# Kernel optimization log

Measured on AMD Instinct MI355X. Metric: run time of the kernel, lower is better.

Reference implementation:

```python
import jax, jax.numpy as jnp
import numpy as np

N, E = 50000, 800000
IN_CH, INTER, H1, H2 = 256, 32, 8, 8
C2 = IN_CH // H2  # 32
NEG_SLOPE = 0.2


def setup_inputs() -> dict:
    key = jax.random.key(0)
    ks = jax.random.split(key, 10)
    x = jax.random.normal(ks[0], (N, IN_CH), dtype=jnp.float32)
    edge_index = jax.random.randint(ks[1], (2, E), 0, N, dtype=jnp.int32)
    s = 0.05
    W1 = jax.random.normal(ks[2], (H1 * INTER, IN_CH), dtype=jnp.float32) * s
    att_src1 = jax.random.normal(ks[3], (1, H1, INTER), dtype=jnp.float32) * s
    att_dst1 = jax.random.normal(ks[4], (1, H1, INTER), dtype=jnp.float32) * s
    b1 = jnp.zeros((H1 * INTER,), dtype=jnp.float32)
    W2 = jax.random.normal(ks[5], (H2 * C2, H1 * INTER), dtype=jnp.float32) * s
    att_src2 = jax.random.normal(ks[6], (1, H2, C2), dtype=jnp.float32) * s
    att_dst2 = jax.random.normal(ks[7], (1, H2, C2), dtype=jnp.float32) * s
    b2 = jnp.zeros((H2 * C2,), dtype=jnp.float32)
    return {"x": x, "edge_index": edge_index,
            "W1": W1, "att_src1": att_src1, "att_dst1": att_dst1, "b1": b1,
            "W2": W2, "att_src2": att_src2, "att_dst2": att_dst2, "b2": b2}


def gat_conv(x, edge_index, W, att_src, att_dst, bias, H, C):
    # PyG GATConv (shared lin for src/dst, add_self_loops=False, concat=True)
    n = x.shape[0]
    src, dst = edge_index[0], edge_index[1]
    xw = (x @ W.T).reshape(n, H, C)                     # [N,H,C]
    a_src = jnp.sum(xw * att_src, axis=-1)              # [N,H]
    a_dst = jnp.sum(xw * att_dst, axis=-1)              # [N,H]
    e = a_src[src] + a_dst[dst]                         # [E,H]
    e = jnp.where(e >= 0, e, NEG_SLOPE * e)             # LeakyReLU(0.2)
    # segment softmax over edges grouped by destination node
    m = jax.ops.segment_max(e, dst, num_segments=n)     # [N,H]
    ex = jnp.exp(e - m[dst])
    denom = jax.ops.segment_sum(ex, dst, num_segments=n)
    alpha = ex / (denom[dst] + 1e-16)                   # [E,H]
    # weighted scatter-aggregate of source messages
    msg = xw[src] * alpha[:, :, None]                   # [E,H,C]
    out = jax.ops.segment_sum(msg, dst, num_segments=n) # [N,H,C]
    return out.reshape(n, H * C) + bias


def reference(x, edge_index, W1, att_src1, att_dst1, b1, W2, att_src2, att_dst2, b2):
    h = gat_conv(x, edge_index, W1, att_src1, att_dst1, b1, H1, INTER)
    h = jax.nn.gelu(h, approximate=False)  # F.gelu default is exact
    h = gat_conv(h, edge_index, W2, att_src2, att_dst2, b2, H2, C2)
    return h[-1]  # eval-path super node
```

## Files before the change

### kernel.cpp

```cpp
#include <hip/hip_runtime.h>
#include <math.h>

#define N_NODES 50000
#define N_EDGES 800000
#define TGT     (N_NODES - 1)
#define C2MAX   256
#define KCAP    258
#define ELMAX   256
#define ROWS    (ELMAX + 1)
#define PBLK    8
#define SCANBLK 512
#define BCAP    8
#define BMWORDS 1568

struct WS {
  int* blkcnt2;
  int* blkbuf2;
  int* cnt2;
  int* fin_k;
  int* gfin;
  int* g_uniq;
  int* g_slot;
  int* g_misc;
  int* l1src;
  float* W1T4;
  float* W2T4;
  float* g_xw2;
  float* g_as2;
  float* g_ad2;
  float* g_as1;
  float* g_ad1;
  float* g_xw1;
};
__host__ __device__ inline WS carve(char* ws) {
  WS w; int* p = (int*)ws;
  w.blkcnt2 = p; p += SCANBLK;
  w.blkbuf2 = p; p += SCANBLK * BCAP;
  w.cnt2 = p;    p += 272;
  w.fin_k = p;   p += 272;
  w.gfin = p;    p += 16;
  w.g_uniq = p;  p += 272;
  w.g_slot = p;  p += C2MAX;
  w.g_misc = p;  p += 16;
  w.l1src = p;   p += KCAP * ELMAX;
  float* f = (float*)p;
  w.W1T4 = f;   f += 65536;
  w.W2T4 = f;   f += 65536;
  w.g_xw2 = f;  f += KCAP * 256;
  w.g_as2 = f;  f += KCAP * 8;
  w.g_ad2 = f;  f += KCAP * 8;
  w.g_as1 = f;  f += KCAP * ROWS * 8;
  w.g_ad1 = f;  f += KCAP * ROWS * 8;
  w.g_xw1 = f;
  return w;
}

__global__ __launch_bounds__(256) void k_scan2(const int* __restrict__ eidx,
    const float* __restrict__ W1, const float* __restrict__ W2, char* ws) {
  WS w = carve(ws);
  int t = threadIdx.x;
  __shared__ float lds[64][65];
  __shared__ int s_list[BCAP];
  __shared__ int s_n;
  if (t == 0) s_n = 0;
  if (blockIdx.x == 0)
    for (int i = t; i < 272 + 272 + 16; i += 256) w.cnt2[i] = 0;
  if (blockIdx.x < 32) {
    int m  = blockIdx.x >> 4;
    int ti = (blockIdx.x >> 2) & 3, tj = blockIdx.x & 3;
    const float* src = m ? W2 : W1;
    float*       dst = m ? w.W2T4 : w.W1T4;
    int r0 = t >> 6, cc = t & 63;
    float tmp[16];
#pragma unroll
    for (int p = 0; p < 16; ++p)
      tmp[p] = src[(ti * 64 + p * 4 + r0) * 256 + tj * 64 + cc];
#pragma unroll
    for (int p = 0; p < 16; ++p)
      lds[p * 4 + r0][cc] = tmp[p];
    __syncthreads();
    int c40 = t >> 6, o = t & 63;
#pragma unroll
    for (int p2 = 0; p2 < 4; ++p2) {
      int c4l = p2 * 4 + c40;
      float4 v = make_float4(lds[o][4 * c4l + 0], lds[o][4 * c4l + 1],
                             lds[o][4 * c4l + 2], lds[o][4 * c4l + 3]);
      ((float4*)dst)[(tj * 16 + c4l) * 256 + ti * 64 + o] = v;
    }
  }
  __syncthreads();
  int tid = blockIdx.x * 256 + t;
  int nthreads = gridDim.x * 256;
  const int* esrc = eidx;
  const int4* edst4 = (const int4*)(eidx + N_EDGES);
  for (int i = tid; i < N_EDGES / 4; i += nthreads) {
    int4 d = edst4[i];
    int dv[4] = {d.x, d.y, d.z, d.w};
#pragma unroll
    for (int j = 0; j < 4; ++j)
      if (dv[j] == TGT) {
        int p = atomicAdd(&s_n, 1);
        if (p < BCAP) s_list[p] = esrc[4 * i + j];
      }
  }
  __syncthreads();
  int n = min(s_n, BCAP);
  if (t == 0) w.blkcnt2[blockIdx.x] = n;
  if (t < n)  w.blkbuf2[blockIdx.x * BCAP + t] = s_list[t];
}

__global__ __launch_bounds__(256) void k_scan1(const int* __restrict__ eidx, char* ws) {
  WS w = carve(ws);
  int t = threadIdx.x;
  __shared__ int s_counts[SCANBLK];
  __shared__ int s_e[C2MAX], s_scan[256], s_uniq[KCAP], s_slot[C2MAX], s_kv[3];
  __shared__ unsigned s_bm[BMWORDS];
  for (int b = t; b < SCANBLK; b += 256) s_counts[b] = min(w.blkcnt2[b], BCAP);
  __syncthreads();
  for (int r = 0; r < SCANBLK / 256; ++r) {
    int b = r * 256 + t;
    int off = 0;
    for (int q = 0; q < b; ++q) off += s_counts[q];
    int n = s_counts[b];
    for (int j = 0; j < n; ++j)
      if (off + j < C2MAX) s_e[off + j] = w.blkbuf2[b * BCAP + j];
    if (b == SCANBLK - 1) s_kv[2] = min(off + n, C2MAX);
  }
  __syncthreads();
  int c2 = s_kv[2];
  int firstIdx = t;
  if (t < c2) {
    int s = s_e[t];
    for (int q = 0; q < t; ++q) if (s_e[q] == s) { firstIdx = q; break; }
  }
  s_scan[t] = (t < c2 && firstIdx == t) ? 1 : 0;
  __syncthreads();
  for (int off = 1; off < 256; off <<= 1) {
    int add = (t >= off) ? s_scan[t - off] : 0;
    __syncthreads();
    s_scan[t] += add;
    __syncthreads();
  }
  if (t < c2 && firstIdx == t) s_uniq[s_scan[t] - 1] = s_e[t];
  __syncthreads();
  if (t < c2) s_slot[t] = s_scan[firstIdx] - 1;
  if (t == 0) {
    int K1 = (c2 > 0) ? s_scan[255] : 0;
    int kd = -1;
    for (int i = 0; i < K1; ++i) if (s_uniq[i] == TGT) { kd = i; break; }
    if (kd < 0) { s_uniq[K1] = TGT; kd = K1; K1++; }
    s_kv[0] = K1; s_kv[1] = kd;
  }
  for (int i = t; i < BMWORDS; i += 256) s_bm[i] = 0u;
  __syncthreads();
  int K1 = s_kv[0];
  for (int i = t; i < K1; i += 256) {
    int u = s_uniq[i];
    atomicOr(&s_bm[u >> 5], 1u << (u & 31));
  }
  if (blockIdx.x == 0) {
    for (int i = t; i < K1; i += 256) w.g_uniq[i] = s_uniq[i];
    if (t < c2) w.g_slot[t] = s_slot[t];
    if (t == 0) { w.g_misc[0] = K1; w.g_misc[1] = s_kv[1]; w.g_misc[2] = c2; }
  }
  __syncthreads();
  int tid = blockIdx.x * 256 + t;
  int nthreads = gridDim.x * 256;
  const int* esrc = eidx;
  const int4* edst4 = (const int4*)(eidx + N_EDGES);
  for (int i = tid; i < N_EDGES / 4; i += nthreads) {
    int4 d = edst4[i];
    int dv[4] = {d.x, d.y, d.z, d.w};
#pragma unroll
    for (int j = 0; j < 4; ++j) {
      int u = dv[j];
      if ((s_bm[u >> 5] >> (u & 31)) & 1u) {
        int k = 0;
        for (int q = 0; q < K1; ++q) if (s_uniq[q] == u) { k = q; break; }
        int p = atomicAdd(&w.cnt2[k], 1);
        if (p < ELMAX) w.l1src[k * ELMAX + p] = esrc[4 * i + j];
      }
    }
  }
}

__global__ __launch_bounds__(256) void k_fused(const float* __restrict__ x,
    const float* __restrict__ aS1, const float* __restrict__ aD1,
    const float* __restrict__ b1, const float* __restrict__ aS2,
    const float* __restrict__ aD2, const float* __restrict__ b2,
    float* __restrict__ out, char* ws) {
  WS w = carve(ws);
  int K1 = w.g_misc[0];
  int k = blockIdx.x;
  if (k >= K1) return;
  int t = threadIdx.x;
  int ne = min(w.cnt2[k], ELMAX);
  int items = ne + 1;
  int myNode = w.g_uniq[k];
  __shared__ __align__(16) float s_xsT[4 * 256];
  __shared__ float s_redS[4 * 256], s_redD[4 * 256];
  __shared__ float s_as[ROWS * 8];
  __shared__ float s_p[ELMAX * 8];
  __shared__ float s_den[8];
  __shared__ __align__(16) float s_h1[256];
  __shared__ int   s_sl[C2MAX];
  __shared__ int   s_win;
  const float4* W1v = (const float4*)w.W1T4;
  const float4* W2v = (const float4*)w.W2T4;
  const float4* xsT4 = (const float4*)s_xsT;

  for (int b = blockIdx.y; b * 4 < items; b += PBLK) {
    int base = b * 4;
    int na = min(4, items - base);
    int nd[4];
#pragma unroll
    for (int i = 0; i < 4; ++i) {
      int it = base + i;
      nd[i] = (it < ne) ? w.l1src[k * ELMAX + it] : myNode;
    }
#pragma unroll
    for (int i = 0; i < 4; ++i)
      s_xsT[t * 4 + i] = x[(size_t)nd[i] * 256 + t];
    __syncthreads();
    float a0 = 0.f, a1 = 0.f, a2 = 0.f, a3 = 0.f;
    for (int cc = 0; cc < 64; cc += 8) {
      float4 wreg[8];
#pragma unroll
      for (int j = 0; j < 8; ++j)
        wreg[j] = W1v[(size_t)(cc + j) * 256 + t];
#pragma unroll
      for (int j = 0; j < 8; ++j) {
        float4 wv = wreg[j];
        int c4 = cc + j;
        float4 x0 = xsT4[4 * c4 + 0];
        float4 x1 = xsT4[4 * c4 + 1];
        float4 x2 = xsT4[4 * c4 + 2];
        float4 x3 = xsT4[4 * c4 + 3];
        a0 = fmaf(wv.x, x0.x, a0); a0 = fmaf(wv.y, x1.x, a0); a0 = fmaf(wv.z, x2.x, a0); a0 = fmaf(wv.w, x3.x, a0);
        a1 = fmaf(wv.x, x0.y, a1); a1 = fmaf(wv.y, x1.y, a1); a1 = fmaf(wv.z, x2.y, a1); a1 = fmaf(wv.w, x3.y, a1);
        a2 = fmaf(wv.x, x0.z, a2); a2 = fmaf(wv.y, x1.z, a2); a2 = fmaf(wv.z, x2.z, a2); a2 = fmaf(wv.w, x3.z, a2);
        a3 = fmaf(wv.x, x0.w, a3); a3 = fmaf(wv.y, x1.w, a3); a3 = fmaf(wv.z, x2.w, a3); a3 = fmaf(wv.w, x3.w, a3);
      }
    }
    float accs[4] = {a0, a1, a2, a3};
    for (int i = 0; i < na; ++i) {
      int it = base + i;
      int row = k * ROWS + it;
      if (it < ne)
        w.g_xw1[(size_t)row * 256 + t] = accs[i];
      s_redS[i * 256 + t] = accs[i] * aS1[t];
      s_redD[i * 256 + t] = accs[i] * aD1[t];
    }
    __syncthreads();
    if (t < 32) {
      int i = t >> 3, h = t & 7;
      if (i < na) {
        float s = 0.f, dd = 0.f;
        for (int q = 0; q < 32; ++q) {
          s  += s_redS[i * 256 + h * 32 + q];
          dd += s_redD[i * 256 + h * 32 + q];
        }
        int row = k * ROWS + base + i;
        w.g_as1[row * 8 + h] = s;
        w.g_ad1[row * 8 + h] = dd;
      }
    }
    __syncthreads();
  }

  __syncthreads();
  if (t == 0) {
    __threadfence();
    int old = __hip_atomic_fetch_add(&w.fin_k[k], 1, __ATOMIC_ACQ_REL, __HIP_MEMORY_SCOPE_AGENT);
    s_win = (old == PBLK - 1);
  }
  __syncthreads();
  if (!s_win) return;
  __threadfence();

  for (int i = t; i < items * 8; i += 256) s_as[i] = w.g_as1[(size_t)(k * ROWS) * 8 + i];
  __syncthreads();
  if (t < 8) {
    int h = t;
    float adst = w.g_ad1[(size_t)(k * ROWS + ne) * 8 + h];
    float m = -INFINITY;
    for (int j = 0; j < ne; ++j) {
      float e = s_as[j * 8 + h] + adst;
      e = (e >= 0.f) ? e : 0.2f * e;
      m = fmaxf(m, e);
    }
    float den = 0.f;
    for (int j = 0; j < ne; ++j) {
      float e = s_as[j * 8 + h] + adst;
      e = (e >= 0.f) ? e : 0.2f * e;
      float p = expf(e - m);
      s_p[j * 8 + h] = p;
      den += p;
    }
    s_den[h] = den + 1e-16f;
  }
  __syncthreads();
  int h = t >> 5;
  float acc = 0.f;
  const float* xwb = w.g_xw1 + (size_t)(k * ROWS) * 256 + t;
  for (int j0 = 0; j0 < ne; j0 += 8) {
    float tmp[8];
#pragma unroll
    for (int j = 0; j < 8; ++j)
      tmp[j] = (j0 + j < ne) ? xwb[(size_t)(j0 + j) * 256] : 0.f;
#pragma unroll
    for (int j = 0; j < 8; ++j)
      if (j0 + j < ne) acc = fmaf(s_p[(j0 + j) * 8 + h], tmp[j], acc);
  }
  float o = (ne > 0) ? acc / s_den[h] : 0.f;
  o += b1[t];
  s_h1[t] = 0.5f * o * (1.f + erff(o * 0.70710678118654752440f));
  __syncthreads();
  float a2s = 0.f;
  const float4* h1v = (const float4*)s_h1;
  for (int cc = 0; cc < 64; cc += 8) {
    float4 wreg[8];
#pragma unroll
    for (int j = 0; j < 8; ++j)
      wreg[j] = W2v[(size_t)(cc + j) * 256 + t];
#pragma unroll
    for (int j = 0; j < 8; ++j) {
      float4 wv = wreg[j];
      float4 hv = h1v[cc + j];
      a2s = fmaf(wv.x, hv.x, a2s); a2s = fmaf(wv.y, hv.y, a2s);
      a2s = fmaf(wv.z, hv.z, a2s); a2s = fmaf(wv.w, hv.w, a2s);
    }
  }
  w.g_xw2[k * 256 + t] = a2s;
  s_redS[t] = a2s * aS2[t];
  s_redD[t] = a2s * aD2[t];
  __syncthreads();
  if (t < 8) {
    float s = 0.f, dd = 0.f;
    for (int q = 0; q < 32; ++q) { s += s_redS[t * 32 + q]; dd += s_redD[t * 32 + q]; }
    w.g_as2[k * 8 + t] = s;
    w.g_ad2[k * 8 + t] = dd;
  }

  __syncthreads();
  if (t == 0) {
    __threadfence();
    int old = __hip_atomic_fetch_add(&w.gfin[0], 1, __ATOMIC_ACQ_REL, __HIP_MEMORY_SCOPE_AGENT);
    s_win = (old == K1 - 1);
  }
  __syncthreads();
  if (!s_win) return;
  __threadfence();

  int c2 = min(w.g_misc[2], C2MAX);
  int kd = w.g_misc[1];
  for (int j = t; j < c2; j += 256) s_sl[j] = w.g_slot[j];
  __syncthreads();
  if (t < 8) {
    float adst = w.g_ad2[kd * 8 + t];
    float m = -INFINITY;
    for (int j = 0; j < c2; ++j) {
      float e = w.g_as2[s_sl[j] * 8 + t] + adst;
      e = (e >= 0.f) ? e : 0.2f * e;
      m = fmaxf(m, e);
    }
    float den = 0.f;
    for (int j = 0; j < c2; ++j) {
      float e = w.g_as2[s_sl[j] * 8 + t] + adst;
      e = (e >= 0.f) ? e : 0.2f * e;
      float p = expf(e - m);
      s_p[j * 8 + t] = p;
      den += p;
    }
    s_den[t] = den + 1e-16f;
  }
  __syncthreads();
  float acc2 = 0.f;
  for (int j0 = 0; j0 < c2; j0 += 8) {
    float tmp[8];
#pragma unroll
    for (int j = 0; j < 8; ++j)
      tmp[j] = (j0 + j < c2) ? w.g_xw2[s_sl[j0 + j] * 256 + t] : 0.f;
#pragma unroll
    for (int j = 0; j < 8; ++j)
      if (j0 + j < c2) acc2 = fmaf(s_p[(j0 + j) * 8 + h], tmp[j], acc2);
  }
  float o2 = (c2 > 0) ? acc2 / s_den[h] : 0.f;
  out[t] = o2 + b2[t];
}

extern "C" void kernel_launch(void* const* d_in, const int* in_sizes, int n_in,
                              void* d_out, int out_size, void* d_ws, size_t ws_size,
                              hipStream_t stream) {
  const float* x    = (const float*)d_in[0];
  const int*   eidx = (const int*)d_in[1];
  const float* W1   = (const float*)d_in[2];
  const float* aS1  = (const float*)d_in[3];
  const float* aD1  = (const float*)d_in[4];
  const float* b1   = (const float*)d_in[5];
  const float* W2   = (const float*)d_in[6];
  const float* aS2  = (const float*)d_in[7];
  const float* aD2  = (const float*)d_in[8];
  const float* b2   = (const float*)d_in[9];
  float* out = (float*)d_out;
  char*  ws  = (char*)d_ws;

  k_scan2<<<SCANBLK, 256, 0, stream>>>(eidx, W1, W2, ws);
  k_scan1<<<SCANBLK, 256, 0, stream>>>(eidx, ws);
  k_fused<<<dim3(KCAP, PBLK), 256, 0, stream>>>(x, aS1, aD1, b1, aS2, aD2, b2, out, ws);
}
```

Baseline: 138.0 us.

## Shrink fused grid, parallel-scan block offsets, pad finish counters, relax atomics

Halves the scan grid to 256 blocks with a larger per-block buffer and replaces the serial per-thread prefix sum over block counts with a shared-memory parallel scan. It also shrinks the fused kernel grid from 258x8 to 96x5, pads the per-k finish counters to separate cache lines, and switches the completion atomics to relaxed ordering while keeping the explicit fences. The smaller grid only stays correct if the kernel loops over k beyond the grid size, which is not visible. The unguarded g_xw1 store writes padding rows, and relaxed atomics rely on the surrounding threadfences for ordering.

```diff
diff --git a/kernel.cpp b/kernel.cpp
--- a/kernel.cpp
+++ b/kernel.cpp
@@ -6,11 +6,13 @@
 #define TGT     (N_NODES - 1)
 #define C2MAX   256
 #define KCAP    258
+#define KGRID   96
 #define ELMAX   256
 #define ROWS    (ELMAX + 1)
-#define PBLK    8
-#define SCANBLK 512
-#define BCAP    8
+#define PBLK    5
+#define FINSTR  16
+#define SCANBLK 256
+#define BCAP    12
 #define BMWORDS 1568
 
 struct WS {
@@ -37,7 +39,7 @@
   w.blkcnt2 = p; p += SCANBLK;
   w.blkbuf2 = p; p += SCANBLK * BCAP;
   w.cnt2 = p;    p += 272;
-  w.fin_k = p;   p += 272;
+  w.fin_k = p;   p += KGRID * FINSTR;
   w.gfin = p;    p += 16;
   w.g_uniq = p;  p += 272;
   w.g_slot = p;  p += C2MAX;
@@ -54,6 +56,7 @@
   w.g_xw1 = f;
   return w;
 }
+#define NZERO (272 + KGRID * FINSTR + 16)
 
 __global__ __launch_bounds__(256) void k_scan2(const int* __restrict__ eidx,
     const float* __restrict__ W1, const float* __restrict__ W2, char* ws) {
@@ -64,7 +67,7 @@
   __shared__ int s_n;
   if (t == 0) s_n = 0;
   if (blockIdx.x == 0)
-    for (int i = t; i < 272 + 272 + 16; i += 256) w.cnt2[i] = 0;
+    for (int i = t; i < NZERO; i += 256) w.cnt2[i] = 0;
   if (blockIdx.x < 32) {
     int m  = blockIdx.x >> 4;
     int ti = (blockIdx.x >> 2) & 3, tj = blockIdx.x & 3;
@@ -112,19 +115,24 @@
 __global__ __launch_bounds__(256) void k_scan1(const int* __restrict__ eidx, char* ws) {
   WS w = carve(ws);
   int t = threadIdx.x;
-  __shared__ int s_counts[SCANBLK];
+  __shared__ int s_counts[SCANBLK], s_coff[SCANBLK];
   __shared__ int s_e[C2MAX], s_scan[256], s_uniq[KCAP], s_slot[C2MAX], s_kv[3];
   __shared__ unsigned s_bm[BMWORDS];
-  for (int b = t; b < SCANBLK; b += 256) s_counts[b] = min(w.blkcnt2[b], BCAP);
-  __syncthreads();
-  for (int r = 0; r < SCANBLK / 256; ++r) {
-    int b = r * 256 + t;
-    int off = 0;
-    for (int q = 0; q < b; ++q) off += s_counts[q];
-    int n = s_counts[b];
+  s_counts[t] = min(w.blkcnt2[t], BCAP);
+  s_coff[t] = s_counts[t];
+  __syncthreads();
+  for (int off = 1; off < SCANBLK; off <<= 1) {
+    int add = (t >= off) ? s_coff[t - off] : 0;
+    __syncthreads();
+    s_coff[t] += add;
+    __syncthreads();
+  }
+  {
+    int n = s_counts[t];
+    int off = s_coff[t] - n;
     for (int j = 0; j < n; ++j)
-      if (off + j < C2MAX) s_e[off + j] = w.blkbuf2[b * BCAP + j];
-    if (b == SCANBLK - 1) s_kv[2] = min(off + n, C2MAX);
+      if (off + j < C2MAX) s_e[off + j] = w.blkbuf2[t * BCAP + j];
+    if (t == 0) s_kv[2] = min(s_coff[SCANBLK - 1], C2MAX);
   }
   __syncthreads();
   int c2 = s_kv[2];
@@ -244,10 +252,8 @@
     }
     float accs[4] = {a0, a1, a2, a3};
     for (int i = 0; i < na; ++i) {
-      int it = base + i;
-      int row = k * ROWS + it;
-      if (it < ne)
-        w.g_xw1[(size_t)row * 256 + t] = accs[i];
+      int row = k * ROWS + base + i;
+      w.g_xw1[(size_t)row * 256 + t] = accs[i];
       s_redS[i * 256 + t] = accs[i] * aS1[t];
       s_redD[i * 256 + t] = accs[i] * aD1[t];
     }
@@ -271,7 +277,8 @@
   __syncthreads();
   if (t == 0) {
     __threadfence();
-    int old = __hip_atomic_fetch_add(&w.fin_k[k], 1, __ATOMIC_ACQ_REL, __HIP_MEMORY_SCOPE_AGENT);
+    int old = __hip_atomic_fetch_add(&w.fin_k[k * FINSTR], 1,
+                                     __ATOMIC_RELAXED, __HIP_MEMORY_SCOPE_AGENT);
     s_win = (old == PBLK - 1);
   }
   __syncthreads();
@@ -345,7 +352,8 @@
   __syncthreads();
   if (t == 0) {
     __threadfence();
-    int old = __hip_atomic_fetch_add(&w.gfin[0], 1, __ATOMIC_ACQ_REL, __HIP_MEMORY_SCOPE_AGENT);
+    int old = __hip_atomic_fetch_add(&w.gfin[0], 1,
+                                     __ATOMIC_RELAXED, __HIP_MEMORY_SCOPE_AGENT);
     s_win = (old == K1 - 1);
   }
   __syncthreads();
@@ -407,5 +415,5 @@
 
   k_scan2<<<SCANBLK, 256, 0, stream>>>(eidx, W1, W2, ws);
   k_scan1<<<SCANBLK, 256, 0, stream>>>(eidx, ws);
-  k_fused<<<dim3(KCAP, PBLK), 256, 0, stream>>>(x, aS1, aD1, b1, aS2, aD2, b2, out, ws);
+  k_fused<<<dim3(KGRID, PBLK), 256, 0, stream>>>(x, aS1, aD1, b1, aS2, aD2, b2, out, ws);
 }
```

Measured after the change: 142.5 us. +3.3%, slower.
